# Kernel tuning notes

Hardware: AMD Instinct MI355X
Metric: run time of the kernel (lower is better)

Reference implementation:

```python
import jax, jax.numpy as jnp
import numpy as np

N_NODES = 50000
N_EDGES = 500000
F_IN = 16      # node feature dim F
F_OUT = 16     # channels F_
E_FEAT = 8     # edge feature dim
HIDDEN = 32    # kernel_network hidden size


def _glorot(key, shape):
    fan_in, fan_out = shape[0], shape[1]
    lim = np.sqrt(6.0 / (fan_in + fan_out)).astype(np.float32)
    return jax.random.uniform(key, shape, jnp.float32, -lim, lim)


def setup_inputs() -> dict:
    key = jax.random.key(0)
    ks = jax.random.split(key, 8)
    x = jax.random.normal(ks[0], (N_NODES, F_IN), jnp.float32)
    e = jax.random.uniform(ks[1], (N_EDGES, E_FEAT), jnp.float32)
    idx_i = jax.random.randint(ks[2], (N_EDGES,), 0, N_NODES, jnp.int32)  # targets
    idx_j = jax.random.randint(ks[3], (N_EDGES,), 0, N_NODES, jnp.int32)  # sources
    W1 = _glorot(ks[4], (E_FEAT, HIDDEN))
    b1 = jnp.zeros((HIDDEN,), jnp.float32)
    W2 = _glorot(ks[5], (HIDDEN, F_OUT * F_IN))
    b2 = jnp.zeros((F_OUT * F_IN,), jnp.float32)
    root_kernel = _glorot(ks[6], (F_IN, F_OUT))
    bias = jnp.zeros((F_OUT,), jnp.float32)
    return {"x": x, "e": e, "idx_i": idx_i, "idx_j": idx_j,
            "W1": W1, "b1": b1, "W2": W2, "b2": b2,
            "root_kernel": root_kernel, "bias": bias}


def reference(x, e, idx_i, idx_j, W1, b1, W2, b2, root_kernel, bias):
    # Edge-conditioned filter-generating network (MLP, relu hidden, linear out)
    h = jax.nn.relu(e @ W1 + b1)                       # [E, HIDDEN]
    kern = (h @ W2 + b2).reshape(-1, F_IN, F_OUT)      # [E, F, F_]
    # gather source node features, per-edge matmul, scatter-add to targets
    msg = jnp.einsum('ef,efc->ec', x[idx_j], kern)     # [E, F_]
    out = jax.ops.segment_sum(msg, idx_i, num_segments=N_NODES)  # [N, F_]
    out = out + x @ root_kernel + bias
    return out
```

## Files before the change

kernel.cpp:

```cpp
#include <hip/hip_runtime.h>

typedef __attribute__((ext_vector_type(8))) _Float16 f16x8_t;
typedef __attribute__((ext_vector_type(2))) _Float16 f16x2_t;
typedef __attribute__((ext_vector_type(4))) float f32x4_t;

__device__ __forceinline__ f16x2_t pkh(float lo, float hi) {
    return __builtin_bit_cast(f16x2_t, __builtin_amdgcn_cvt_pkrtz(lo, hi));
}
__device__ __forceinline__ unsigned int pkrtz(float lo, float hi) {
    return __builtin_bit_cast(unsigned int, __builtin_amdgcn_cvt_pkrtz(lo, hi));
}

#define LD4(p) (*reinterpret_cast<const float4*>(p))


__global__ __launch_bounds__(256) void prep_kernel(
    const float* __restrict__ x,
    const float* __restrict__ W1,
    const float* __restrict__ b1,
    const float* __restrict__ W2,
    const float* __restrict__ b2,
    const float* __restrict__ rootk,
    const float* __restrict__ bias,
    float* __restrict__ out,
    _Float16* __restrict__ tab,
    int n_nodes, int root_blocks)
{
    const int tid = threadIdx.x;
    const int bid = blockIdx.x;

    if (bid < root_blocks) {
        __shared__ float sR[256];
        __shared__ float sB[16];
        if (tid < 256) sR[tid] = rootk[tid];
        if (tid < 16)  sB[tid] = bias[tid];
        __syncthreads();

        int nid = bid * 256 + tid;
        if (nid >= n_nodes) return;

        const float* xp = x + (size_t)nid * 16;
        float xf[16];
#pragma unroll
        for (int f = 0; f < 16; f += 4) {
            float4 v = LD4(xp + f);
            xf[f] = v.x; xf[f + 1] = v.y; xf[f + 2] = v.z; xf[f + 3] = v.w;
        }
        float o[16];
#pragma unroll
        for (int cc = 0; cc < 16; ++cc) o[cc] = sB[cc];
#pragma unroll
        for (int f = 0; f < 16; ++f) {
            float p = xf[f];
#pragma unroll
            for (int cc = 0; cc < 16; ++cc)
                o[cc] = fmaf(p, sR[f * 16 + cc], o[cc]);
        }
        float* dst = out + (size_t)nid * 16;
#pragma unroll
        for (int cc = 0; cc < 16; cc += 4)
            *reinterpret_cast<float4*>(dst + cc) = make_float4(o[cc], o[cc+1], o[cc+2], o[cc+3]);
    } else {
        for (int it = tid; it < 64 * 19; it += 256) {
            int grp  = it >> 6;
            int lane = it & 63;
            int q = lane >> 4, cc = lane & 15;
            union { _Float16 h[8]; uint4 u; } pk;
            if (grp < 2) {
                int hh = grp;
#pragma unroll
                for (int j = 0; j < 8; ++j) {
                    float v = 0.f;
                    if (q == 0)              v = W1[j * 32 + cc + 16 * hh];
                    else if (q == 1 && j==0) v = b1[cc + 16 * hh];
                    pk.h[j] = (_Float16)v;
                }
                *reinterpret_cast<uint4*>(tab + ((size_t)hh * 64 + lane) * 8) = pk.u;
            } else {
                int s = grp - 2;
#pragma unroll
                for (int j = 0; j < 8; ++j) {
                    float v;
                    if (s < 16) {
                        int hd = (j < 4) ? (4 * q + j) : (4 * q + 12 + j);
                        v = W2[hd * 256 + s * 16 + cc];
                    } else {
                        v = (q < 2) ? b2[(q * 8 + j) * 16 + cc] : 0.f;
                    }
                    pk.h[j] = (_Float16)v;
                }
                *reinterpret_cast<uint4*>(tab + 1024 + ((size_t)s * 64 + lane) * 8) = pk.u;
            }
        }
    }
}

__device__ __forceinline__ float4 shfl4(float4 v, int src) {
    float4 r;
    r.x = __shfl(v.x, src); r.y = __shfl(v.y, src);
    r.z = __shfl(v.z, src); r.w = __shfl(v.w, src);
    return r;
}

template<int EXACT>
__global__ __launch_bounds__(256) void edge_mfma_kernel(
    const float* __restrict__ x,
    const float* __restrict__ efeat,
    const int*   __restrict__ idx_i,
    const int*   __restrict__ idx_j,
    const _Float16* __restrict__ tab,
    float* __restrict__ out,
    int n_edges, int n_groups)
{
    const int lane = threadIdx.x & 63;
    const int q = lane >> 4;
    const int c = lane & 15;

    const f16x8_t* w1f = reinterpret_cast<const f16x8_t*>(tab) + lane;
    const f16x8_t aW1_0 = w1f[0];
    const f16x8_t aW1_1 = w1f[64];
    const f16x8_t* w2f = reinterpret_cast<const f16x8_t*>(tab + 1024) + lane;
    f16x8_t bW2[17];
#pragma unroll
    for (int s = 0; s < 17; ++s) bW2[s] = w2f[s * 64];

    const unsigned int c1 = (q == 1) ? 0x00003C00u : 0u;
    const bool isq0 = (q == 0);
    const bool qodd = (q & 1);
    float* const outc = out + c;

    const int wid = blockIdx.x * 4 + (threadIdx.x >> 6);
    const int g0  = wid * 4;
    if (g0 >= n_groups) return;
    const int rem = n_groups - g0;

    auto ldj = [&](int gg) -> int {
        int eid = gg * 16 + c;
        if (!EXACT) { if (eid >= n_edges) eid = n_edges - 1; }
        return idx_j[eid];
    };
    auto eptr = [&](int gg) -> const float* {
        int eid = gg * 16 + c;
        if (!EXACT) { if (eid >= n_edges) eid = n_edges - 1; }
        return efeat + (size_t)eid * 8;
    };

    auto compute = [&](float4 XQ, float4 E0, float4 E1, int gg) {
        int t0, t1, t2, t3;
        if (EXACT || (gg * 16 + 16 <= n_edges)) {
            int4 tv = *reinterpret_cast<const int4*>(idx_i + gg * 16 + q * 4);
            t0 = tv.x; t1 = tv.y; t2 = tv.z; t3 = tv.w;
        } else {
            const int eb = gg * 16 + q * 4;
            t0 = (eb + 0 < n_edges) ? idx_i[eb + 0] : 0;
            t1 = (eb + 1 < n_edges) ? idx_i[eb + 1] : 0;
            t2 = (eb + 2 < n_edges) ? idx_i[eb + 2] : 0;
            t3 = (eb + 3 < n_edges) ? idx_i[eb + 3] : 0;
        }

        float4 X0 = shfl4(XQ, c);
        float4 X1 = shfl4(XQ, c + 16);
        float4 X2 = shfl4(XQ, c + 32);
        float4 X3 = shfl4(XQ, c + 48);

        union { f16x8_t v8; f16x2_t v2[4]; unsigned int u[4]; } bB;
        bB.u[0] = isq0 ? pkrtz(E0.x, E0.y) : c1;
        bB.u[1] = isq0 ? pkrtz(E0.z, E0.w) : 0u;
        bB.u[2] = isq0 ? pkrtz(E1.x, E1.y) : 0u;
        bB.u[3] = isq0 ? pkrtz(E1.z, E1.w) : 0u;

        f32x4_t z4 = {0.f, 0.f, 0.f, 0.f};
        f32x4_t h0 = __builtin_amdgcn_mfma_f32_16x16x32_f16(aW1_0, bB.v8, z4, 0, 0, 0);
        f32x4_t h1 = __builtin_amdgcn_mfma_f32_16x16x32_f16(aW1_1, bB.v8, z4, 0, 0, 0);

        f16x2_t hp0 = pkh(fmaxf(h0[0], 0.f), fmaxf(h0[1], 0.f));
        f16x2_t hp1 = pkh(fmaxf(h0[2], 0.f), fmaxf(h0[3], 0.f));
        f16x2_t hp2 = pkh(fmaxf(h1[0], 0.f), fmaxf(h1[1], 0.f));
        f16x2_t hp3 = pkh(fmaxf(h1[2], 0.f), fmaxf(h1[3], 0.f));

        float xf[16];
        xf[0]=X0.x; xf[1]=X0.y; xf[2]=X0.z; xf[3]=X0.w;
        xf[4]=X1.x; xf[5]=X1.y; xf[6]=X1.z; xf[7]=X1.w;
        xf[8]=X2.x; xf[9]=X2.y; xf[10]=X2.z; xf[11]=X2.w;
        xf[12]=X3.x; xf[13]=X3.y; xf[14]=X3.z; xf[15]=X3.w;

        f16x2_t xss[16];
#pragma unroll
        for (int f = 0; f < 16; ++f)
            xss[f] = pkh(xf[f], xf[f]);

        union { f16x8_t v8; unsigned int u[4]; } xb;
        xb.u[0] = pkrtz(qodd ? xf[8]  : xf[0], qodd ? xf[9]  : xf[1]);
        xb.u[1] = pkrtz(qodd ? xf[10] : xf[2], qodd ? xf[11] : xf[3]);
        xb.u[2] = pkrtz(qodd ? xf[12] : xf[4], qodd ? xf[13] : xf[5]);
        xb.u[3] = pkrtz(qodd ? xf[14] : xf[6], qodd ? xf[15] : xf[7]);

        f32x4_t acc0 = {0.f, 0.f, 0.f, 0.f};
        f32x4_t acc1 = {0.f, 0.f, 0.f, 0.f};
        union { f16x8_t v8; f16x2_t v2[4]; } afr;
#pragma unroll
        for (int s = 0; s < 16; s += 2) {
            f16x2_t xs2 = xss[s];
            afr.v2[0] = hp0 * xs2;
            afr.v2[1] = hp1 * xs2;
            afr.v2[2] = hp2 * xs2;
            afr.v2[3] = hp3 * xs2;
            acc0 = __builtin_amdgcn_mfma_f32_16x16x32_f16(afr.v8, bW2[s], acc0, 0, 0, 0);
            xs2 = xss[s + 1];
            afr.v2[0] = hp0 * xs2;
            afr.v2[1] = hp1 * xs2;
            afr.v2[2] = hp2 * xs2;
            afr.v2[3] = hp3 * xs2;
            acc1 = __builtin_amdgcn_mfma_f32_16x16x32_f16(afr.v8, bW2[s + 1], acc1, 0, 0, 0);
        }
        acc0 = __builtin_amdgcn_mfma_f32_16x16x32_f16(xb.v8, bW2[16], acc0, 0, 0, 0);

        const float rr0 = acc0[0] + acc1[0];
        const float rr1 = acc0[1] + acc1[1];
        const float rr2 = acc0[2] + acc1[2];
        const float rr3 = acc0[3] + acc1[3];
        if (EXACT) {
            atomicAdd(outc + (size_t)t0 * 16, rr0);
            atomicAdd(outc + (size_t)t1 * 16, rr1);
            atomicAdd(outc + (size_t)t2 * 16, rr2);
            atomicAdd(outc + (size_t)t3 * 16, rr3);
        } else {
            const int eb = gg * 16 + q * 4;
            if (eb + 0 < n_edges) atomicAdd(outc + (size_t)t0 * 16, rr0);
            if (eb + 1 < n_edges) atomicAdd(outc + (size_t)t1 * 16, rr1);
            if (eb + 2 < n_edges) atomicAdd(outc + (size_t)t2 * 16, rr2);
            if (eb + 3 < n_edges) atomicAdd(outc + (size_t)t3 * 16, rr3);
        }
    };

#define STAGE(BXQ, BE0, BE1, jv, gg)                                \
    {                                                               \
        BXQ = LD4(x + (size_t)(jv) * 16 + q * 4);                   \
        const float* ep = eptr(gg);                                 \
        BE0 = LD4(ep); BE1 = LD4(ep + 4);                           \
    }

    const int jA = ldj(g0);
    const int jB = (rem > 1) ? ldj(g0 + 1) : 0;
    const int jC = (rem > 2) ? ldj(g0 + 2) : 0;
    const int jD = (rem > 3) ? ldj(g0 + 3) : 0;

    float4 aq, ae0, ae1;
    float4 bq, be0, be1;

    STAGE(aq, ae0, ae1, jA, g0);
    if (rem > 1) STAGE(bq, be0, be1, jB, g0 + 1);
    compute(aq, ae0, ae1, g0);
    if (rem > 1) {
        if (rem > 2) STAGE(aq, ae0, ae1, jC, g0 + 2);
        compute(bq, be0, be1, g0 + 1);
        if (rem > 2) {
            if (rem > 3) STAGE(bq, be0, be1, jD, g0 + 3);
            compute(aq, ae0, ae1, g0 + 2);
            if (rem > 3) compute(bq, be0, be1, g0 + 3);
        }
    }
#undef STAGE
}

extern "C" void kernel_launch(void* const* d_in, const int* in_sizes, int n_in,
                              void* d_out, int out_size, void* d_ws, size_t ws_size,
                              hipStream_t stream) {
    const float* x     = (const float*)d_in[0];
    const float* e     = (const float*)d_in[1];
    const int*   idx_i = (const int*)d_in[2];
    const int*   idx_j = (const int*)d_in[3];
    const float* W1    = (const float*)d_in[4];
    const float* b1    = (const float*)d_in[5];
    const float* W2    = (const float*)d_in[6];
    const float* b2    = (const float*)d_in[7];
    const float* rootk = (const float*)d_in[8];
    const float* bias  = (const float*)d_in[9];

    int n_nodes  = in_sizes[0] / 16;
    int n_edges  = in_sizes[2];
    int n_groups = (n_edges + 15) / 16;

    float* out = (float*)d_out;
    _Float16* tab = (_Float16*)d_ws;

    int root_blocks = (n_nodes + 255) / 256;
    prep_kernel<<<root_blocks + 1, 256, 0, stream>>>(x, W1, b1, W2, b2, rootk, bias,
                                                     out, tab, n_nodes, root_blocks);

    int blocks = (n_groups + 15) / 16;
    if ((n_edges & 15) == 0)
        edge_mfma_kernel<1><<<blocks, 256, 0, stream>>>(x, e, idx_i, idx_j, tab, out,
                                                        n_edges, n_groups);
    else
        edge_mfma_kernel<0><<<blocks, 256, 0, stream>>>(x, e, idx_i, idx_j, tab, out,
                                                        n_edges, n_groups);
}
```

Before: 46.22 us.

## Load per-wave edge indices and features coalesced once, distribute via shuffles

Each wave now loads idx_j, idx_i and edge features for all 64 of its edges with one coalesced per-lane load, then hands them to the 16-lane groups through cross-lane shuffles. All four x gathers are issued up front rather than software-pipelined in pairs. The x values are packed to fp16 once and broadcast into the half2 multiplier with byte-permute ops, replacing the per-feature conversions. Atomics are deferred to the end, which keeps 16 result registers live and adds shuffle traffic in exchange for fewer, wider memory requests.

```diff
diff --git a/kernel.cpp b/kernel.cpp
--- a/kernel.cpp
+++ b/kernel.cpp
@@ -10,8 +10,21 @@
 __device__ __forceinline__ unsigned int pkrtz(float lo, float hi) {
     return __builtin_bit_cast(unsigned int, __builtin_amdgcn_cvt_pkrtz(lo, hi));
 }
+__device__ __forceinline__ f16x2_t dup_lo(unsigned int u) {
+    return __builtin_bit_cast(f16x2_t, __builtin_amdgcn_perm(u, u, 0x01000100u));
+}
+__device__ __forceinline__ f16x2_t dup_hi(unsigned int u) {
+    return __builtin_bit_cast(f16x2_t, __builtin_amdgcn_perm(u, u, 0x03020302u));
+}
 
 #define LD4(p) (*reinterpret_cast<const float4*>(p))
+
+__device__ __forceinline__ float4 shfl4(float4 v, int src) {
+    float4 r;
+    r.x = __shfl(v.x, src); r.y = __shfl(v.y, src);
+    r.z = __shfl(v.z, src); r.w = __shfl(v.w, src);
+    return r;
+}
 
 
 __global__ __launch_bounds__(256) void prep_kernel(
@@ -95,15 +108,8 @@
     }
 }
 
-__device__ __forceinline__ float4 shfl4(float4 v, int src) {
-    float4 r;
-    r.x = __shfl(v.x, src); r.y = __shfl(v.y, src);
-    r.z = __shfl(v.z, src); r.w = __shfl(v.w, src);
-    return r;
-}
-
 template<int EXACT>
-__global__ __launch_bounds__(256) void edge_mfma_kernel(
+__global__ __launch_bounds__(256) void edge_v16_kernel(
     const float* __restrict__ x,
     const float* __restrict__ efeat,
     const int*   __restrict__ idx_i,
@@ -132,43 +138,54 @@
     const int wid = blockIdx.x * 4 + (threadIdx.x >> 6);
     const int g0  = wid * 4;
     if (g0 >= n_groups) return;
-    const int rem = n_groups - g0;
-
-    auto ldj = [&](int gg) -> int {
-        int eid = gg * 16 + c;
-        if (!EXACT) { if (eid >= n_edges) eid = n_edges - 1; }
-        return idx_j[eid];
-    };
-    auto eptr = [&](int gg) -> const float* {
-        int eid = gg * 16 + c;
-        if (!EXACT) { if (eid >= n_edges) eid = n_edges - 1; }
-        return efeat + (size_t)eid * 8;
-    };
-
-    auto compute = [&](float4 XQ, float4 E0, float4 E1, int gg) {
-        int t0, t1, t2, t3;
-        if (EXACT || (gg * 16 + 16 <= n_edges)) {
-            int4 tv = *reinterpret_cast<const int4*>(idx_i + gg * 16 + q * 4);
-            t0 = tv.x; t1 = tv.y; t2 = tv.z; t3 = tv.w;
-        } else {
-            const int eb = gg * 16 + q * 4;
-            t0 = (eb + 0 < n_edges) ? idx_i[eb + 0] : 0;
-            t1 = (eb + 1 < n_edges) ? idx_i[eb + 1] : 0;
-            t2 = (eb + 2 < n_edges) ? idx_i[eb + 2] : 0;
-            t3 = (eb + 3 < n_edges) ? idx_i[eb + 3] : 0;
-        }
-
+    const int rem  = n_groups - g0;
+    const int base = g0 * 16;
+
+    int el = base + lane;
+    if (el >= n_edges) el = n_edges - 1;
+    const int jall = idx_j[el];
+    const int iall = idx_i[el];
+    const float* ep = efeat + (size_t)el * 8;
+    const float4 Eo0 = LD4(ep);
+    const float4 Eo1 = LD4(ep + 4);
+
+    const int js0 = __shfl(jall, c);
+    const float4 XQ0 = LD4(x + (size_t)js0 * 16 + q * 4);
+    float4 XQ1 = XQ0, XQ2 = XQ0, XQ3 = XQ0;
+    if (rem > 1) { int j1 = __shfl(jall, 16 + c); XQ1 = LD4(x + (size_t)j1 * 16 + q * 4); }
+    if (rem > 2) { int j2 = __shfl(jall, 32 + c); XQ2 = LD4(x + (size_t)j2 * 16 + q * 4); }
+    if (rem > 3) { int j3 = __shfl(jall, 48 + c); XQ3 = LD4(x + (size_t)j3 * 16 + q * 4); }
+
+    const unsigned int eo0 = pkrtz(Eo0.x, Eo0.y);
+    const unsigned int eo1 = pkrtz(Eo0.z, Eo0.w);
+    const unsigned int eo2 = pkrtz(Eo1.x, Eo1.y);
+    const unsigned int eo3 = pkrtz(Eo1.z, Eo1.w);
+
+    float rr00=0,rr01=0,rr02=0,rr03=0, rr10=0,rr11=0,rr12=0,rr13=0;
+    float rr20=0,rr21=0,rr22=0,rr23=0, rr30=0,rr31=0,rr32=0,rr33=0;
+
+    auto compute = [&](int k16, float4 XQ, float& o0, float& o1, float& o2, float& o3) {
         float4 X0 = shfl4(XQ, c);
         float4 X1 = shfl4(XQ, c + 16);
         float4 X2 = shfl4(XQ, c + 32);
         float4 X3 = shfl4(XQ, c + 48);
 
-        union { f16x8_t v8; f16x2_t v2[4]; unsigned int u[4]; } bB;
-        bB.u[0] = isq0 ? pkrtz(E0.x, E0.y) : c1;
-        bB.u[1] = isq0 ? pkrtz(E0.z, E0.w) : 0u;
-        bB.u[2] = isq0 ? pkrtz(E1.x, E1.y) : 0u;
-        bB.u[3] = isq0 ? pkrtz(E1.z, E1.w) : 0u;
-
+        unsigned int pr0 = pkrtz(X0.x, X0.y), pr1 = pkrtz(X0.z, X0.w);
+        unsigned int pr2 = pkrtz(X1.x, X1.y), pr3 = pkrtz(X1.z, X1.w);
+        unsigned int pr4 = pkrtz(X2.x, X2.y), pr5 = pkrtz(X2.z, X2.w);
+        unsigned int pr6 = pkrtz(X3.x, X3.y), pr7 = pkrtz(X3.z, X3.w);
+
+        union { f16x8_t v8; unsigned int u[4]; } bB;
+        {
+            unsigned int u0 = __shfl(eo0, k16 + c);
+            unsigned int u1 = __shfl(eo1, k16 + c);
+            unsigned int u2 = __shfl(eo2, k16 + c);
+            unsigned int u3 = __shfl(eo3, k16 + c);
+            bB.u[0] = isq0 ? u0 : c1;
+            bB.u[1] = isq0 ? u1 : 0u;
+            bB.u[2] = isq0 ? u2 : 0u;
+            bB.u[3] = isq0 ? u3 : 0u;
+        }
         f32x4_t z4 = {0.f, 0.f, 0.f, 0.f};
         f32x4_t h0 = __builtin_amdgcn_mfma_f32_16x16x32_f16(aW1_0, bB.v8, z4, 0, 0, 0);
         f32x4_t h1 = __builtin_amdgcn_mfma_f32_16x16x32_f16(aW1_1, bB.v8, z4, 0, 0, 0);
@@ -178,89 +195,71 @@
         f16x2_t hp2 = pkh(fmaxf(h1[0], 0.f), fmaxf(h1[1], 0.f));
         f16x2_t hp3 = pkh(fmaxf(h1[2], 0.f), fmaxf(h1[3], 0.f));
 
-        float xf[16];
-        xf[0]=X0.x; xf[1]=X0.y; xf[2]=X0.z; xf[3]=X0.w;
-        xf[4]=X1.x; xf[5]=X1.y; xf[6]=X1.z; xf[7]=X1.w;
-        xf[8]=X2.x; xf[9]=X2.y; xf[10]=X2.z; xf[11]=X2.w;
-        xf[12]=X3.x; xf[13]=X3.y; xf[14]=X3.z; xf[15]=X3.w;
-
-        f16x2_t xss[16];
-#pragma unroll
-        for (int f = 0; f < 16; ++f)
-            xss[f] = pkh(xf[f], xf[f]);
-
         union { f16x8_t v8; unsigned int u[4]; } xb;
-        xb.u[0] = pkrtz(qodd ? xf[8]  : xf[0], qodd ? xf[9]  : xf[1]);
-        xb.u[1] = pkrtz(qodd ? xf[10] : xf[2], qodd ? xf[11] : xf[3]);
-        xb.u[2] = pkrtz(qodd ? xf[12] : xf[4], qodd ? xf[13] : xf[5]);
-        xb.u[3] = pkrtz(qodd ? xf[14] : xf[6], qodd ? xf[15] : xf[7]);
+        xb.u[0] = qodd ? pr4 : pr0;
+        xb.u[1] = qodd ? pr5 : pr1;
+        xb.u[2] = qodd ? pr6 : pr2;
+        xb.u[3] = qodd ? pr7 : pr3;
 
         f32x4_t acc0 = {0.f, 0.f, 0.f, 0.f};
         f32x4_t acc1 = {0.f, 0.f, 0.f, 0.f};
         union { f16x8_t v8; f16x2_t v2[4]; } afr;
-#pragma unroll
-        for (int s = 0; s < 16; s += 2) {
-            f16x2_t xs2 = xss[s];
-            afr.v2[0] = hp0 * xs2;
-            afr.v2[1] = hp1 * xs2;
-            afr.v2[2] = hp2 * xs2;
-            afr.v2[3] = hp3 * xs2;
-            acc0 = __builtin_amdgcn_mfma_f32_16x16x32_f16(afr.v8, bW2[s], acc0, 0, 0, 0);
-            xs2 = xss[s + 1];
-            afr.v2[0] = hp0 * xs2;
-            afr.v2[1] = hp1 * xs2;
-            afr.v2[2] = hp2 * xs2;
-            afr.v2[3] = hp3 * xs2;
-            acc1 = __builtin_amdgcn_mfma_f32_16x16x32_f16(afr.v8, bW2[s + 1], acc1, 0, 0, 0);
+        unsigned int prs[8] = {pr0, pr1, pr2, pr3, pr4, pr5, pr6, pr7};
+#pragma unroll
+        for (int s2 = 0; s2 < 8; ++s2) {
+            const unsigned int pp = prs[s2];
+            f16x2_t xlo = dup_lo(pp);
+            afr.v2[0] = hp0 * xlo;
+            afr.v2[1] = hp1 * xlo;
+            afr.v2[2] = hp2 * xlo;
+            afr.v2[3] = hp3 * xlo;
+            acc0 = __builtin_amdgcn_mfma_f32_16x16x32_f16(afr.v8, bW2[2 * s2], acc0, 0, 0, 0);
+            f16x2_t xhi = dup_hi(pp);
+            afr.v2[0] = hp0 * xhi;
+            afr.v2[1] = hp1 * xhi;
+            afr.v2[2] = hp2 * xhi;
+            afr.v2[3] = hp3 * xhi;
+            acc1 = __builtin_amdgcn_mfma_f32_16x16x32_f16(afr.v8, bW2[2 * s2 + 1], acc1, 0, 0, 0);
         }
         acc0 = __builtin_amdgcn_mfma_f32_16x16x32_f16(xb.v8, bW2[16], acc0, 0, 0, 0);
 
-        const float rr0 = acc0[0] + acc1[0];
-        const float rr1 = acc0[1] + acc1[1];
-        const float rr2 = acc0[2] + acc1[2];
-        const float rr3 = acc0[3] + acc1[3];
-        if (EXACT) {
-            atomicAdd(outc + (size_t)t0 * 16, rr0);
-            atomicAdd(outc + (size_t)t1 * 16, rr1);
-            atomicAdd(outc + (size_t)t2 * 16, rr2);
-            atomicAdd(outc + (size_t)t3 * 16, rr3);
-        } else {
-            const int eb = gg * 16 + q * 4;
-            if (eb + 0 < n_edges) atomicAdd(outc + (size_t)t0 * 16, rr0);
-            if (eb + 1 < n_edges) atomicAdd(outc + (size_t)t1 * 16, rr1);
-            if (eb + 2 < n_edges) atomicAdd(outc + (size_t)t2 * 16, rr2);
-            if (eb + 3 < n_edges) atomicAdd(outc + (size_t)t3 * 16, rr3);
-        }
+        o0 = acc0[0] + acc1[0];
+        o1 = acc0[1] + acc1[1];
+        o2 = acc0[2] + acc1[2];
+        o3 = acc0[3] + acc1[3];
     };
 
-#define STAGE(BXQ, BE0, BE1, jv, gg)                                \
-    {                                                               \
-        BXQ = LD4(x + (size_t)(jv) * 16 + q * 4);                   \
-        const float* ep = eptr(gg);                                 \
-        BE0 = LD4(ep); BE1 = LD4(ep + 4);                           \
+    compute(0, XQ0, rr00, rr01, rr02, rr03);
+    if (rem > 1) compute(16, XQ1, rr10, rr11, rr12, rr13);
+    if (rem > 2) compute(32, XQ2, rr20, rr21, rr22, rr23);
+    if (rem > 3) compute(48, XQ3, rr30, rr31, rr32, rr33);
+
+    const int qr = q * 4;
+#define SCATTER(k16, R0, R1, R2, R3)                                          \
+    {                                                                         \
+        int t0 = __shfl(iall, (k16) + qr + 0);                                \
+        int t1 = __shfl(iall, (k16) + qr + 1);                                \
+        int t2 = __shfl(iall, (k16) + qr + 2);                                \
+        int t3 = __shfl(iall, (k16) + qr + 3);                                \
+        if (EXACT) {                                                          \
+            atomicAdd(outc + (size_t)t0 * 16, R0);                            \
+            atomicAdd(outc + (size_t)t1 * 16, R1);                            \
+            atomicAdd(outc + (size_t)t2 * 16, R2);                            \
+            atomicAdd(outc + (size_t)t3 * 16, R3);                            \
+        } else {                                                              \
+            const int eb = base + (k16) + qr;                                 \
+            if (eb + 0 < n_edges) atomicAdd(outc + (size_t)t0 * 16, R0);      \
+            if (eb + 1 < n_edges) atomicAdd(outc + (size_t)t1 * 16, R1);      \
+            if (eb + 2 < n_edges) atomicAdd(outc + (size_t)t2 * 16, R2);      \
+            if (eb + 3 < n_edges) atomicAdd(outc + (size_t)t3 * 16, R3);      \
+        }                                                                     \
     }
 
-    const int jA = ldj(g0);
-    const int jB = (rem > 1) ? ldj(g0 + 1) : 0;
-    const int jC = (rem > 2) ? ldj(g0 + 2) : 0;
-    const int jD = (rem > 3) ? ldj(g0 + 3) : 0;
-
-    float4 aq, ae0, ae1;
-    float4 bq, be0, be1;
-
-    STAGE(aq, ae0, ae1, jA, g0);
-    if (rem > 1) STAGE(bq, be0, be1, jB, g0 + 1);
-    compute(aq, ae0, ae1, g0);
-    if (rem > 1) {
-        if (rem > 2) STAGE(aq, ae0, ae1, jC, g0 + 2);
-        compute(bq, be0, be1, g0 + 1);
-        if (rem > 2) {
-            if (rem > 3) STAGE(bq, be0, be1, jD, g0 + 3);
-            compute(aq, ae0, ae1, g0 + 2);
-            if (rem > 3) compute(bq, be0, be1, g0 + 3);
-        }
-    }
-#undef STAGE
+    SCATTER(0, rr00, rr01, rr02, rr03);
+    if (rem > 1) SCATTER(16, rr10, rr11, rr12, rr13);
+    if (rem > 2) SCATTER(32, rr20, rr21, rr22, rr23);
+    if (rem > 3) SCATTER(48, rr30, rr31, rr32, rr33);
+#undef SCATTER
 }
 
 extern "C" void kernel_launch(void* const* d_in, const int* in_sizes, int n_in,
@@ -288,11 +287,12 @@
     prep_kernel<<<root_blocks + 1, 256, 0, stream>>>(x, W1, b1, W2, b2, rootk, bias,
                                                      out, tab, n_nodes, root_blocks);
 
-    int blocks = (n_groups + 15) / 16;
+    int waves  = (n_groups + 3) / 4;
+    int blocks = (waves + 3) / 4;
     if ((n_edges & 15) == 0)
-        edge_mfma_kernel<1><<<blocks, 256, 0, stream>>>(x, e, idx_i, idx_j, tab, out,
-                                                        n_edges, n_groups);
+        edge_v16_kernel<1><<<blocks, 256, 0, stream>>>(x, e, idx_i, idx_j, tab, out,
+                                                       n_edges, n_groups);
     else
-        edge_mfma_kernel<0><<<blocks, 256, 0, stream>>>(x, e, idx_i, idx_j, tab, out,
-                                                        n_edges, n_groups);
-}
+        edge_v16_kernel<0><<<blocks, 256, 0, stream>>>(x, e, idx_i, idx_j, tab, out,
+                                                       n_edges, n_groups);
+}
```

After: 48.32 us. 4.5% more time.

## Replace atomic scatter with bucketed per-node gather of materialized edge messages

Applied to the files above, without the earlier changes.

Edge messages are written densely to a workspace buffer instead of being atomically added to the output. A bucket kernel records each edge's index into fixed per-target slots, with an overflow list handled by atomics. A gather kernel then sums each node's messages. The edge kernel also changes from per-wave prefetch staging with shuffles to a grid-stride loop with direct 16-float loads. This adds several kernels and roughly 32 MB of message traffic in exchange for removing contended float atomics.

```diff
diff --git a/kernel.cpp b/kernel.cpp
--- a/kernel.cpp
+++ b/kernel.cpp
@@ -3,6 +3,9 @@
 typedef __attribute__((ext_vector_type(8))) _Float16 f16x8_t;
 typedef __attribute__((ext_vector_type(2))) _Float16 f16x2_t;
 typedef __attribute__((ext_vector_type(4))) float f32x4_t;
+
+#define SLOTS 64
+#define OVF_CAP 8192
 
 __device__ __forceinline__ f16x2_t pkh(float lo, float hi) {
     return __builtin_bit_cast(f16x2_t, __builtin_amdgcn_cvt_pkrtz(lo, hi));
@@ -24,6 +27,8 @@
     const float* __restrict__ bias,
     float* __restrict__ out,
     _Float16* __restrict__ tab,
+    int* __restrict__ cnt,
+    int* __restrict__ ovf_cnt,
     int n_nodes, int root_blocks)
 {
     const int tid = threadIdx.x;
@@ -38,6 +43,7 @@
 
         int nid = bid * 256 + tid;
         if (nid >= n_nodes) return;
+        if (cnt) cnt[nid] = 0;
 
         const float* xp = x + (size_t)nid * 16;
         float xf[16];
@@ -61,6 +67,7 @@
         for (int cc = 0; cc < 16; cc += 4)
             *reinterpret_cast<float4*>(dst + cc) = make_float4(o[cc], o[cc+1], o[cc+2], o[cc+3]);
     } else {
+        if (tid == 0 && ovf_cnt) *ovf_cnt = 0;
         for (int it = tid; it < 64 * 19; it += 256) {
             int grp  = it >> 6;
             int lane = it & 63;
@@ -95,20 +102,34 @@
     }
 }
 
-__device__ __forceinline__ float4 shfl4(float4 v, int src) {
-    float4 r;
-    r.x = __shfl(v.x, src); r.y = __shfl(v.y, src);
-    r.z = __shfl(v.z, src); r.w = __shfl(v.w, src);
-    return r;
-}
-
-template<int EXACT>
+__global__ __launch_bounds__(256) void bucket_kernel(
+    const int* __restrict__ idx_i,
+    int* __restrict__ cnt,
+    int* __restrict__ eord,
+    int* __restrict__ ovf_cnt,
+    int* __restrict__ ovf,
+    int n_edges)
+{
+    int e = blockIdx.x * 256 + threadIdx.x;
+    if (e >= n_edges) return;
+    int t = idx_i[e];
+    int pos = atomicAdd(cnt + t, 1);
+    if (pos < SLOTS) {
+        eord[(size_t)t * SLOTS + pos] = e;
+    } else {
+        int o = atomicAdd(ovf_cnt, 1);
+        if (o < OVF_CAP) ovf[o] = e;
+    }
+}
+
+template<int MSG, int EXACT>
 __global__ __launch_bounds__(256) void edge_mfma_kernel(
     const float* __restrict__ x,
     const float* __restrict__ efeat,
     const int*   __restrict__ idx_i,
     const int*   __restrict__ idx_j,
     const _Float16* __restrict__ tab,
+    float* __restrict__ msg,
     float* __restrict__ out,
     int n_edges, int n_groups)
 {
@@ -127,48 +148,24 @@
     const unsigned int c1 = (q == 1) ? 0x00003C00u : 0u;
     const bool isq0 = (q == 0);
     const bool qodd = (q & 1);
-    float* const outc = out + c;
-
-    const int wid = blockIdx.x * 4 + (threadIdx.x >> 6);
-    const int g0  = wid * 4;
-    if (g0 >= n_groups) return;
-    const int rem = n_groups - g0;
-
-    auto ldj = [&](int gg) -> int {
-        int eid = gg * 16 + c;
-        if (!EXACT) { if (eid >= n_edges) eid = n_edges - 1; }
-        return idx_j[eid];
-    };
-    auto eptr = [&](int gg) -> const float* {
-        int eid = gg * 16 + c;
-        if (!EXACT) { if (eid >= n_edges) eid = n_edges - 1; }
-        return efeat + (size_t)eid * 8;
-    };
-
-    auto compute = [&](float4 XQ, float4 E0, float4 E1, int gg) {
-        int t0, t1, t2, t3;
-        if (EXACT || (gg * 16 + 16 <= n_edges)) {
-            int4 tv = *reinterpret_cast<const int4*>(idx_i + gg * 16 + q * 4);
-            t0 = tv.x; t1 = tv.y; t2 = tv.z; t3 = tv.w;
-        } else {
-            const int eb = gg * 16 + q * 4;
-            t0 = (eb + 0 < n_edges) ? idx_i[eb + 0] : 0;
-            t1 = (eb + 1 < n_edges) ? idx_i[eb + 1] : 0;
-            t2 = (eb + 2 < n_edges) ? idx_i[eb + 2] : 0;
-            t3 = (eb + 3 < n_edges) ? idx_i[eb + 3] : 0;
-        }
-
-        float4 X0 = shfl4(XQ, c);
-        float4 X1 = shfl4(XQ, c + 16);
-        float4 X2 = shfl4(XQ, c + 32);
-        float4 X3 = shfl4(XQ, c + 48);
-
-        union { f16x8_t v8; f16x2_t v2[4]; unsigned int u[4]; } bB;
+
+    const int nwaves = gridDim.x * 4;
+    for (int g = blockIdx.x * 4 + (threadIdx.x >> 6); g < n_groups; g += nwaves) {
+        int eid = g * 16 + c;
+        bool va = (eid < n_edges);
+        int el = va ? eid : (n_edges - 1);
+        int j = idx_j[el];
+
+        const float* xp = x + (size_t)j * 16;
+        float4 X0 = LD4(xp), X1 = LD4(xp + 4), X2 = LD4(xp + 8), X3 = LD4(xp + 12);
+        const float* ep = efeat + (size_t)el * 8;
+        float4 E0 = LD4(ep), E1 = LD4(ep + 4);
+
+        union { f16x8_t v8; unsigned int u[4]; } bB;
         bB.u[0] = isq0 ? pkrtz(E0.x, E0.y) : c1;
         bB.u[1] = isq0 ? pkrtz(E0.z, E0.w) : 0u;
         bB.u[2] = isq0 ? pkrtz(E1.x, E1.y) : 0u;
         bB.u[3] = isq0 ? pkrtz(E1.z, E1.w) : 0u;
-
         f32x4_t z4 = {0.f, 0.f, 0.f, 0.f};
         f32x4_t h0 = __builtin_amdgcn_mfma_f32_16x16x32_f16(aW1_0, bB.v8, z4, 0, 0, 0);
         f32x4_t h1 = __builtin_amdgcn_mfma_f32_16x16x32_f16(aW1_1, bB.v8, z4, 0, 0, 0);
@@ -183,11 +180,14 @@
         xf[4]=X1.x; xf[5]=X1.y; xf[6]=X1.z; xf[7]=X1.w;
         xf[8]=X2.x; xf[9]=X2.y; xf[10]=X2.z; xf[11]=X2.w;
         xf[12]=X3.x; xf[13]=X3.y; xf[14]=X3.z; xf[15]=X3.w;
+        if (!EXACT && !va) {
+#pragma unroll
+            for (int t = 0; t < 16; ++t) xf[t] = 0.f;
+        }
 
         f16x2_t xss[16];
 #pragma unroll
-        for (int f = 0; f < 16; ++f)
-            xss[f] = pkh(xf[f], xf[f]);
+        for (int f = 0; f < 16; ++f) xss[f] = pkh(xf[f], xf[f]);
 
         union { f16x8_t v8; unsigned int u[4]; } xb;
         xb.u[0] = pkrtz(qodd ? xf[8]  : xf[0], qodd ? xf[9]  : xf[1]);
@@ -195,22 +195,17 @@
         xb.u[2] = pkrtz(qodd ? xf[12] : xf[4], qodd ? xf[13] : xf[5]);
         xb.u[3] = pkrtz(qodd ? xf[14] : xf[6], qodd ? xf[15] : xf[7]);
 
-        f32x4_t acc0 = {0.f, 0.f, 0.f, 0.f};
-        f32x4_t acc1 = {0.f, 0.f, 0.f, 0.f};
+        f32x4_t acc0 = {0.f,0.f,0.f,0.f}, acc1 = {0.f,0.f,0.f,0.f};
         union { f16x8_t v8; f16x2_t v2[4]; } afr;
 #pragma unroll
         for (int s = 0; s < 16; s += 2) {
             f16x2_t xs2 = xss[s];
-            afr.v2[0] = hp0 * xs2;
-            afr.v2[1] = hp1 * xs2;
-            afr.v2[2] = hp2 * xs2;
-            afr.v2[3] = hp3 * xs2;
+            afr.v2[0] = hp0 * xs2; afr.v2[1] = hp1 * xs2;
+            afr.v2[2] = hp2 * xs2; afr.v2[3] = hp3 * xs2;
             acc0 = __builtin_amdgcn_mfma_f32_16x16x32_f16(afr.v8, bW2[s], acc0, 0, 0, 0);
             xs2 = xss[s + 1];
-            afr.v2[0] = hp0 * xs2;
-            afr.v2[1] = hp1 * xs2;
-            afr.v2[2] = hp2 * xs2;
-            afr.v2[3] = hp3 * xs2;
+            afr.v2[0] = hp0 * xs2; afr.v2[1] = hp1 * xs2;
+            afr.v2[2] = hp2 * xs2; afr.v2[3] = hp3 * xs2;
             acc1 = __builtin_amdgcn_mfma_f32_16x16x32_f16(afr.v8, bW2[s + 1], acc1, 0, 0, 0);
         }
         acc0 = __builtin_amdgcn_mfma_f32_16x16x32_f16(xb.v8, bW2[16], acc0, 0, 0, 0);
@@ -219,48 +214,74 @@
         const float rr1 = acc0[1] + acc1[1];
         const float rr2 = acc0[2] + acc1[2];
         const float rr3 = acc0[3] + acc1[3];
-        if (EXACT) {
-            atomicAdd(outc + (size_t)t0 * 16, rr0);
-            atomicAdd(outc + (size_t)t1 * 16, rr1);
-            atomicAdd(outc + (size_t)t2 * 16, rr2);
-            atomicAdd(outc + (size_t)t3 * 16, rr3);
+        const int eb = g * 16 + q * 4;
+
+        if (MSG) {
+            float* mp = msg + (size_t)eb * 16 + c;
+            if (EXACT || (eb + 0 < n_edges)) mp[0]  = rr0;
+            if (EXACT || (eb + 1 < n_edges)) mp[16] = rr1;
+            if (EXACT || (eb + 2 < n_edges)) mp[32] = rr2;
+            if (EXACT || (eb + 3 < n_edges)) mp[48] = rr3;
         } else {
-            const int eb = gg * 16 + q * 4;
-            if (eb + 0 < n_edges) atomicAdd(outc + (size_t)t0 * 16, rr0);
-            if (eb + 1 < n_edges) atomicAdd(outc + (size_t)t1 * 16, rr1);
-            if (eb + 2 < n_edges) atomicAdd(outc + (size_t)t2 * 16, rr2);
-            if (eb + 3 < n_edges) atomicAdd(outc + (size_t)t3 * 16, rr3);
-        }
-    };
-
-#define STAGE(BXQ, BE0, BE1, jv, gg)                                \
-    {                                                               \
-        BXQ = LD4(x + (size_t)(jv) * 16 + q * 4);                   \
-        const float* ep = eptr(gg);                                 \
-        BE0 = LD4(ep); BE1 = LD4(ep + 4);                           \
-    }
-
-    const int jA = ldj(g0);
-    const int jB = (rem > 1) ? ldj(g0 + 1) : 0;
-    const int jC = (rem > 2) ? ldj(g0 + 2) : 0;
-    const int jD = (rem > 3) ? ldj(g0 + 3) : 0;
-
-    float4 aq, ae0, ae1;
-    float4 bq, be0, be1;
-
-    STAGE(aq, ae0, ae1, jA, g0);
-    if (rem > 1) STAGE(bq, be0, be1, jB, g0 + 1);
-    compute(aq, ae0, ae1, g0);
-    if (rem > 1) {
-        if (rem > 2) STAGE(aq, ae0, ae1, jC, g0 + 2);
-        compute(bq, be0, be1, g0 + 1);
-        if (rem > 2) {
-            if (rem > 3) STAGE(bq, be0, be1, jD, g0 + 3);
-            compute(aq, ae0, ae1, g0 + 2);
-            if (rem > 3) compute(bq, be0, be1, g0 + 3);
-        }
-    }
-#undef STAGE
+            int t0 = (EXACT || eb + 0 < n_edges) ? idx_i[eb + 0] : 0;
+            int t1 = (EXACT || eb + 1 < n_edges) ? idx_i[eb + 1] : 0;
+            int t2 = (EXACT || eb + 2 < n_edges) ? idx_i[eb + 2] : 0;
+            int t3 = (EXACT || eb + 3 < n_edges) ? idx_i[eb + 3] : 0;
+            float* outc = out + c;
+            if (EXACT || eb + 0 < n_edges) atomicAdd(outc + (size_t)t0 * 16, rr0);
+            if (EXACT || eb + 1 < n_edges) atomicAdd(outc + (size_t)t1 * 16, rr1);
+            if (EXACT || eb + 2 < n_edges) atomicAdd(outc + (size_t)t2 * 16, rr2);
+            if (EXACT || eb + 3 < n_edges) atomicAdd(outc + (size_t)t3 * 16, rr3);
+        }
+    }
+}
+
+__global__ __launch_bounds__(256) void gather_kernel(
+    const float* __restrict__ msg,
+    const int*   __restrict__ cnt,
+    const int*   __restrict__ eord,
+    float* __restrict__ out,
+    int n_nodes)
+{
+    int gi = blockIdx.x * 256 + threadIdx.x;
+    int n = gi >> 4;
+    int c = gi & 15;
+    if (n >= n_nodes) return;
+
+    int m = cnt[n];
+    m = (m < SLOTS) ? m : SLOTS;
+    const int* ep = eord + (size_t)n * SLOTS;
+
+    float s0 = 0.f, s1 = 0.f;
+    int k = 0;
+    for (; k + 4 <= m; k += 4) {
+        int4 ev = *reinterpret_cast<const int4*>(ep + k);
+        float v0 = msg[(size_t)ev.x * 16 + c];
+        float v1 = msg[(size_t)ev.y * 16 + c];
+        float v2 = msg[(size_t)ev.z * 16 + c];
+        float v3 = msg[(size_t)ev.w * 16 + c];
+        s0 += v0 + v2;
+        s1 += v1 + v3;
+    }
+    for (; k < m; ++k) s0 += msg[(size_t)ep[k] * 16 + c];
+    out[(size_t)n * 16 + c] += s0 + s1;
+}
+
+__global__ __launch_bounds__(256) void ovf_kernel(
+    const float* __restrict__ msg,
+    const int*   __restrict__ idx_i,
+    const int*   __restrict__ ovf_cnt,
+    const int*   __restrict__ ovf,
+    float* __restrict__ out)
+{
+    int m = *ovf_cnt;
+    if (m > OVF_CAP) m = OVF_CAP;
+    for (int it = threadIdx.x + blockIdx.x * 256; it < m * 16; it += gridDim.x * 256) {
+        int o = it >> 4, c = it & 15;
+        int e = ovf[o];
+        int t = idx_i[e];
+        atomicAdd(out + (size_t)t * 16 + c, msg[(size_t)e * 16 + c]);
+    }
 }
 
 extern "C" void kernel_launch(void* const* d_in, const int* in_sizes, int n_in,
@@ -283,16 +304,36 @@
 
     float* out = (float*)d_out;
     _Float16* tab = (_Float16*)d_ws;
+    int* cnt     = (int*)((char*)d_ws + 65536);
+    int* ovf_cnt = (int*)((char*)d_ws + 327680);
+    int* ovf     = (int*)((char*)d_ws + 327744);
+    int* eord    = (int*)((char*)d_ws + 524288);
+    float* msg   = (float*)((char*)d_ws + (16u << 20));
+
+    size_t need = (16u << 20) + (size_t)n_edges * 16 * sizeof(float);
+    const int use_msg = (ws_size >= need &&
+                         524288 + (size_t)n_nodes * SLOTS * 4 <= (16u << 20)) ? 1 : 0;
 
     int root_blocks = (n_nodes + 255) / 256;
     prep_kernel<<<root_blocks + 1, 256, 0, stream>>>(x, W1, b1, W2, b2, rootk, bias,
-                                                     out, tab, n_nodes, root_blocks);
-
-    int blocks = (n_groups + 15) / 16;
-    if ((n_edges & 15) == 0)
-        edge_mfma_kernel<1><<<blocks, 256, 0, stream>>>(x, e, idx_i, idx_j, tab, out,
-                                                        n_edges, n_groups);
-    else
-        edge_mfma_kernel<0><<<blocks, 256, 0, stream>>>(x, e, idx_i, idx_j, tab, out,
-                                                        n_edges, n_groups);
-}
+                                                     out, tab, use_msg ? cnt : nullptr,
+                                                     use_msg ? ovf_cnt : nullptr,
+                                                     n_nodes, root_blocks);
+
+    if (use_msg) {
+        int bblocks = (n_edges + 255) / 256;
+        bucket_kernel<<<bblocks, 256, 0, stream>>>(idx_i, cnt, eord, ovf_cnt, ovf, n_edges);
+        if ((n_edges & 15) == 0)
+            edge_mfma_kernel<1, 1><<<1024, 256, 0, stream>>>(x, e, idx_i, idx_j, tab,
+                                                             msg, out, n_edges, n_groups);
+        else
+            edge_mfma_kernel<1, 0><<<1024, 256, 0, stream>>>(x, e, idx_i, idx_j, tab,
+                                                             msg, out, n_edges, n_groups);
+        int gblocks = (n_nodes * 16 + 255) / 256;
+        gather_kernel<<<gblocks, 256, 0, stream>>>(msg, cnt, eord, out, n_nodes);
+        ovf_kernel<<<32, 256, 0, stream>>>(msg, idx_i, ovf_cnt, ovf, out);
+    } else {
+        edge_mfma_kernel<0, 0><<<1024, 256, 0, stream>>>(x, e, idx_i, idx_j, tab,
+                                                         msg, out, n_edges, n_groups);
+    }
+}
```

Result: slower. 80.77 us (+74.7%).
